# Kernel optimization log

Measured on AMD Instinct MI355X. Metric: run time of the kernel, lower is better.

## Reference

```python
import jax, jax.numpy as jnp
import numpy as np

B, N, DIM = 2, 2048, 512
H, DH = 8, 64            # heads, dim_head; inner_dim = H*DH = 512 == DIM -> to_out is Identity
BAND = 128               # mask keeps -128 <= j-i <= 127
LN_EPS = 1e-5


def _band_mask(n):
    i = jnp.arange(n)
    d = i[None, :] - i[:, None]          # j - i
    return (d >= -BAND) & (d < BAND)     # [n, n] bool


def setup_inputs() -> dict:
    key = jax.random.key(0)
    k1, k2 = jax.random.split(key, 2)
    x = jax.random.normal(k1, (B, N, DIM), dtype=jnp.float32)
    w_qkv = jax.random.normal(k2, (DIM, 3 * H * DH), dtype=jnp.float32) * (DIM ** -0.5)
    gamma = jnp.ones((DIM,), dtype=jnp.float32)
    beta = jnp.zeros((DIM,), dtype=jnp.float32)
    return {"x": x, "w_qkv": w_qkv, "gamma": gamma, "beta": beta}


def reference(x, w_qkv, gamma, beta):
    # LayerNorm
    mu = jnp.mean(x, axis=-1, keepdims=True)
    var = jnp.mean((x - mu) ** 2, axis=-1, keepdims=True)
    xn = (x - mu) * jax.lax.rsqrt(var + LN_EPS) * gamma + beta

    # qkv projection (no bias); split and reshape to [B, H, N, DH]
    qkv = xn @ w_qkv                                   # [B, N, 3*H*DH]
    q, k, v = jnp.split(qkv, 3, axis=-1)
    to_heads = lambda t: t.reshape(B, N, H, DH).transpose(0, 2, 1, 3)
    q, k, v = to_heads(q), to_heads(k), to_heads(v)

    # NOTE: original forward never applies self.scale -> no scaling here (faithful).
    attn = jnp.einsum('bhnd,bhmd->bhnm', q, k)         # [B, H, N, N]
    attn = jnp.where(_band_mask(N), attn, jnp.float32(-10000.0))
    probs = jax.nn.softmax(attn, axis=-1)
    out = jnp.einsum('bhnm,bhmd->bhnd', probs, v)      # [B, H, N, DH]
    out = out.transpose(0, 2, 1, 3).reshape(B, N, H * DH)
    return out  # to_out is Identity since inner_dim == dim
```

## Files before the change

### kernel.cpp

```cpp
#include <hip/hip_runtime.h>
#include <hip/hip_bf16.h>

#define B_    2
#define N_    2048
#define DIM_  512
#define H_    8
#define DH_   64
#define QKVW  1536
#define BAND_ 128
#define LN_EPS 1e-5f

typedef __attribute__((ext_vector_type(8))) short bf16x8;
typedef __attribute__((ext_vector_type(4))) float f32x4;
typedef __attribute__((ext_vector_type(8))) unsigned short ushort8;

__device__ __forceinline__ float bf2f(unsigned short u) {
    union { unsigned int i; float f; } w; w.i = ((unsigned int)u) << 16; return w.f;
}
__device__ __forceinline__ unsigned short f2bf(float f) {
    __hip_bfloat16 h = __float2bfloat16(f);
    return *reinterpret_cast<unsigned short*>(&h);
}
__device__ __forceinline__ void async_copy16(void* lds, const void* g) {
    __builtin_amdgcn_global_load_lds(
        (const __attribute__((address_space(1))) unsigned int*)g,
        (__attribute__((address_space(3))) unsigned int*)lds, 16, 0, 0);
}

__global__ __launch_bounds__(256) void prep_kernel(const float* __restrict__ x,
                                                   const float* __restrict__ gamma,
                                                   const float* __restrict__ beta,
                                                   const float* __restrict__ W,
                                                   unsigned short* __restrict__ xh,
                                                   unsigned short* __restrict__ xl,
                                                   unsigned short* __restrict__ Bh,
                                                   unsigned short* __restrict__ Bl) {
    __shared__ float T[64][65];
    if (blockIdx.x < 1024) {
        const int row  = blockIdx.x * 4 + (threadIdx.x >> 6);
        const int lane = threadIdx.x & 63;
        const float* xr = x + (size_t)row * DIM_ + lane * 8;
        float4 a = *(const float4*)xr;
        float4 c = *(const float4*)(xr + 4);
        float s  = (a.x + a.y) + (a.z + a.w) + (c.x + c.y) + (c.z + c.w);
        float sq = a.x*a.x + a.y*a.y + a.z*a.z + a.w*a.w
                 + c.x*c.x + c.y*c.y + c.z*c.z + c.w*c.w;
        #pragma unroll
        for (int o = 32; o; o >>= 1) { s += __shfl_xor(s, o); sq += __shfl_xor(sq, o); }
        const float mu  = s * (1.0f / DIM_);
        const float var = sq * (1.0f / DIM_) - mu * mu;
        const float rs  = rsqrtf(var + LN_EPS);
        float4 g0 = *(const float4*)(gamma + lane * 8);
        float4 g1 = *(const float4*)(gamma + lane * 8 + 4);
        float4 b0 = *(const float4*)(beta  + lane * 8);
        float4 b1 = *(const float4*)(beta  + lane * 8 + 4);
        const float fv[8] = {
            (a.x - mu) * rs * g0.x + b0.x, (a.y - mu) * rs * g0.y + b0.y,
            (a.z - mu) * rs * g0.z + b0.z, (a.w - mu) * rs * g0.w + b0.w,
            (c.x - mu) * rs * g1.x + b1.x, (c.y - mu) * rs * g1.y + b1.y,
            (c.z - mu) * rs * g1.z + b1.z, (c.w - mu) * rs * g1.w + b1.w };
        ushort8 h, l;
        #pragma unroll
        for (int j = 0; j < 8; ++j) {
            const unsigned short hv = f2bf(fv[j]);
            h[j] = hv; l[j] = f2bf(fv[j] - bf2f(hv));
        }
        *(ushort8*)(xh + (size_t)row * DIM_ + lane * 8) = h;
        *(ushort8*)(xl + (size_t)row * DIM_ + lane * 8) = l;
    } else {
        const int bx = blockIdx.x - 1024;
        const int n0 = (bx % 24) * 64, k0 = (bx / 24) * 64;
        const int tid = threadIdx.x;
        #pragma unroll
        for (int e = 0; e < 4; ++e) {
            const int lin = e * 256 + tid;
            const int kk = lin >> 4;
            const int n4 = (lin & 15) * 4;
            float4 f = *(const float4*)(W + (size_t)(k0 + kk) * QKVW + n0 + n4);
            T[kk][n4 + 0] = f.x; T[kk][n4 + 1] = f.y;
            T[kk][n4 + 2] = f.z; T[kk][n4 + 3] = f.w;
        }
        __syncthreads();
        #pragma unroll
        for (int e = 0; e < 4; ++e) {
            const int lin = e * 256 + tid;
            const int nn = lin >> 4;
            const int kq = (lin & 15) * 4;
            ushort4 h, l;
            float f;
            f = T[kq + 0][nn]; h.x = f2bf(f); l.x = f2bf(f - bf2f(h.x));
            f = T[kq + 1][nn]; h.y = f2bf(f); l.y = f2bf(f - bf2f(h.y));
            f = T[kq + 2][nn]; h.z = f2bf(f); l.z = f2bf(f - bf2f(h.z));
            f = T[kq + 3][nn]; h.w = f2bf(f); l.w = f2bf(f - bf2f(h.w));
            *(ushort4*)(Bh + (size_t)(n0 + nn) * DIM_ + k0 + kq) = h;
            *(ushort4*)(Bl + (size_t)(n0 + nn) * DIM_ + k0 + kq) = l;
        }
    }
}

__global__ __launch_bounds__(256) void gemm_mfma(const unsigned short* __restrict__ Ah,
                                                 const unsigned short* __restrict__ Al,
                                                 const unsigned short* __restrict__ Bh,
                                                 const unsigned short* __restrict__ Bl,
                                                 unsigned short* __restrict__ Qh,
                                                 unsigned short* __restrict__ Ql,
                                                 unsigned short* __restrict__ Kh,
                                                 unsigned short* __restrict__ Kl,
                                                 unsigned short* __restrict__ Vt) {
    __shared__ __attribute__((aligned(16))) unsigned short sAh[64 * 64],  sAl[64 * 64];
    __shared__ __attribute__((aligned(16))) unsigned short sBh[128 * 64], sBl[128 * 64];
    const int tid  = threadIdx.x;
    const int lane = tid & 63, wave = tid >> 6;
    const int wr = wave >> 1, wc = wave & 1;
    const int lg = lane >> 4, l16 = lane & 15;

    const int bid = blockIdx.x;
    const int sb  = (bid & 7) * 96 + (bid >> 3);
    const int row0 = (sb / 12) * 64;
    const int col0 = (sb % 12) * 128;
    const int part = col0 >> 9;

    f32x4 acc[2][4] = {};

    for (int k0 = 0; k0 < DIM_; k0 += 64) {
        __syncthreads();
        #pragma unroll
        for (int e = 0; e < 2; ++e) {
            const int s0  = e * 256 + wave * 64;
            const int idx = s0 + lane;
            const int r   = idx >> 3;
            const int pb  = idx & 7;
            const int klog = pb ^ (r & 7);
            const size_t ga = (size_t)(row0 + r) * DIM_ + k0 + klog * 8;
            async_copy16(&sAh[s0 * 8], Ah + ga);
            if (part < 2) async_copy16(&sAl[s0 * 8], Al + ga);
        }
        #pragma unroll
        for (int e = 0; e < 4; ++e) {
            const int s0  = e * 256 + wave * 64;
            const int idx = s0 + lane;
            const int r   = idx >> 3;
            const int pb  = idx & 7;
            const int klog = pb ^ (r & 7);
            const size_t gb = (size_t)(col0 + r) * DIM_ + k0 + klog * 8;
            async_copy16(&sBh[s0 * 8], Bh + gb);
            if (part < 2) async_copy16(&sBl[s0 * 8], Bl + gb);
        }
        __syncthreads();

        #pragma unroll
        for (int kh = 0; kh < 2; ++kh) {
            bf16x8 ah[2], bh[4];
            #pragma unroll
            for (int mi = 0; mi < 2; ++mi) {
                const int r = wr * 32 + mi * 16 + l16;
                ah[mi] = *(const bf16x8*)&sAh[r * 64 + (((kh * 4 + lg) ^ (r & 7)) * 8)];
            }
            #pragma unroll
            for (int ni = 0; ni < 4; ++ni) {
                const int r = wc * 64 + ni * 16 + l16;
                bh[ni] = *(const bf16x8*)&sBh[r * 64 + (((kh * 4 + lg) ^ (r & 7)) * 8)];
            }
            if (part < 2) {
                bf16x8 al[2], bl[4];
                #pragma unroll
                for (int mi = 0; mi < 2; ++mi) {
                    const int r = wr * 32 + mi * 16 + l16;
                    al[mi] = *(const bf16x8*)&sAl[r * 64 + (((kh * 4 + lg) ^ (r & 7)) * 8)];
                }
                #pragma unroll
                for (int ni = 0; ni < 4; ++ni) {
                    const int r = wc * 64 + ni * 16 + l16;
                    bl[ni] = *(const bf16x8*)&sBl[r * 64 + (((kh * 4 + lg) ^ (r & 7)) * 8)];
                }
                #pragma unroll
                for (int mi = 0; mi < 2; ++mi)
                    #pragma unroll
                    for (int ni = 0; ni < 4; ++ni) {
                        acc[mi][ni] = __builtin_amdgcn_mfma_f32_16x16x32_bf16(ah[mi], bh[ni], acc[mi][ni], 0, 0, 0);
                        acc[mi][ni] = __builtin_amdgcn_mfma_f32_16x16x32_bf16(al[mi], bh[ni], acc[mi][ni], 0, 0, 0);
                        acc[mi][ni] = __builtin_amdgcn_mfma_f32_16x16x32_bf16(ah[mi], bl[ni], acc[mi][ni], 0, 0, 0);
                    }
            } else {
                #pragma unroll
                for (int mi = 0; mi < 2; ++mi)
                    #pragma unroll
                    for (int ni = 0; ni < 4; ++ni)
                        acc[mi][ni] = __builtin_amdgcn_mfma_f32_16x16x32_bf16(ah[mi], bh[ni], acc[mi][ni], 0, 0, 0);
            }
        }
    }

    const int colbase = col0 + wc * 64;
    const int head = (colbase & 511) >> 6;
    if (part < 2) {
        unsigned short* __restrict__ Ih = (part == 0) ? Qh : Kh;
        unsigned short* __restrict__ Il = (part == 0) ? Ql : Kl;
        #pragma unroll
        for (int mi = 0; mi < 2; ++mi) {
            const int rb = row0 + wr * 32 + mi * 16 + lg * 4;
            const int n  = rb & 2047;
            const size_t tbase = ((size_t)((rb >> 11) * H_ + head) * 32 + (n >> 6)) * 4096;
            #pragma unroll
            for (int ni = 0; ni < 4; ++ni) {
                const int d  = ni * 16 + l16;
                const int k8 = d >> 3;
                #pragma unroll
                for (int rr = 0; rr < 4; ++rr) {
                    const int r = (n & 63) + rr;
                    const size_t off = tbase + r * 64 + ((k8 ^ (r & 7)) * 8) + (d & 7);
                    const float v = acc[mi][ni][rr];
                    const unsigned short hv = f2bf(v);
                    Ih[off] = hv;
                    Il[off] = f2bf(v - bf2f(hv));
                }
            }
        }
    } else {
        #pragma unroll
        for (int mi = 0; mi < 2; ++mi) {
            const int rb = row0 + wr * 32 + mi * 16 + lg * 4;
            const int n  = rb & 2047;
            const size_t cbase = ((size_t)((rb >> 11) * H_ + head) * 32 + (n >> 6)) * 4096;
            const int nr = n & 63;
            #pragma unroll
            for (int ni = 0; ni < 4; ++ni) {
                const int d = ni * 16 + l16;
                const size_t off = cbase + d * 64 + (((nr >> 3) ^ (d & 7)) * 8) + (nr & 7);
                ushort4 pk;
                pk.x = f2bf(acc[mi][ni][0]); pk.y = f2bf(acc[mi][ni][1]);
                pk.z = f2bf(acc[mi][ni][2]); pk.w = f2bf(acc[mi][ni][3]);
                *(ushort4*)&Vt[off] = pk;
            }
        }
    }
}

__global__ __launch_bounds__(256) void attn_mfma(const unsigned short* __restrict__ Qh,
                                                 const unsigned short* __restrict__ Ql,
                                                 const unsigned short* __restrict__ Kh,
                                                 const unsigned short* __restrict__ Kl,
                                                 const unsigned short* __restrict__ Vt,
                                                 float* __restrict__ out) {
    const int bid = blockIdx.x;
    const int sb  = (bid & 7) * 64 + (bid >> 3);
    const int tile = sb & 31;
    const int h    = (sb >> 5) & 7;
    const int b    = sb >> 8;
    const int i0   = tile * 64;
    const int tid  = threadIdx.x;
    const int lane = tid & 63, wave = tid >> 6;
    const int lg   = lane >> 4, l16 = lane & 15;

    __shared__ __attribute__((aligned(16))) unsigned short sKh[4096], sKl[4096];
    __shared__ __attribute__((aligned(16))) unsigned short sP[4][1024];

    const size_t hb = (size_t)(b * H_ + h) * 32;

    bf16x8 qh[2], ql[2];
    {
        const int r = wave * 16 + l16;
        const size_t tb = (hb + tile) * 4096;
        #pragma unroll
        for (int kh = 0; kh < 2; ++kh) {
            const size_t off = tb + r * 64 + (((kh * 4 + lg) ^ (r & 7)) * 8);
            qh[kh] = *(const bf16x8*)(Qh + off);
            ql[kh] = *(const bf16x8*)(Ql + off);
        }
    }

    float m_run[4], l_run[4];
    f32x4 oacc[4] = {};
    #pragma unroll
    for (int r = 0; r < 4; ++r) { m_run[r] = -1e30f; l_run[r] = 0.0f; }

    #pragma unroll 1
    for (int c = 0; c < 5; ++c) {
        const int jbase = i0 - 128 + c * 64;
        if (jbase + 64 <= 0 || jbase >= N_) continue;
        __syncthreads();
        const size_t kbG = (hb + (jbase >> 6)) * 4096;
        #pragma unroll
        for (int e = 0; e < 4; ++e) {
            const int s0  = e * 256 + wave * 64;
            const int arr = s0 >> 9;
            const int w0  = (s0 & 511) * 8;
            unsigned short* dst = (arr == 0) ? sKh : sKl;
            const unsigned short* src = (arr == 0) ? Kh : Kl;
            async_copy16(dst + w0, src + kbG + w0 + lane * 8);
        }
        __syncthreads();

        f32x4 sacc[4] = {};
        #pragma unroll
        for (int kh = 0; kh < 2; ++kh) {
            #pragma unroll
            for (int t = 0; t < 4; ++t) {
                const int r = t * 16 + l16;
                const int off = r * 64 + ((((kh * 4 + lg)) ^ (r & 7)) * 8);
                const bf16x8 kbh = *(const bf16x8*)&sKh[off];
                const bf16x8 kbl = *(const bf16x8*)&sKl[off];
                sacc[t] = __builtin_amdgcn_mfma_f32_16x16x32_bf16(qh[kh], kbh, sacc[t], 0, 0, 0);
                sacc[t] = __builtin_amdgcn_mfma_f32_16x16x32_bf16(ql[kh], kbh, sacc[t], 0, 0, 0);
                sacc[t] = __builtin_amdgcn_mfma_f32_16x16x32_bf16(qh[kh], kbl, sacc[t], 0, 0, 0);
            }
        }

        #pragma unroll
        for (int r = 0; r < 4; ++r) {
            const int i = i0 + wave * 16 + lg * 4 + r;
            float sv[4];
            float mx = -1e30f;
            #pragma unroll
            for (int t = 0; t < 4; ++t) {
                const int j = jbase + t * 16 + l16;
                const int d = j - i;
                const bool ok = (d >= -BAND_) && (d < BAND_);
                sv[t] = ok ? sacc[t][r] : -1e30f;
                mx = fmaxf(mx, sv[t]);
            }
            #pragma unroll
            for (int o = 1; o < 16; o <<= 1) mx = fmaxf(mx, __shfl_xor(mx, o));
            const float m_new = fmaxf(m_run[r], mx);
            const float alpha = __expf(m_run[r] - m_new);
            float p[4], lc = 0.f;
            #pragma unroll
            for (int t = 0; t < 4; ++t) { p[t] = __expf(sv[t] - m_new); lc += p[t]; }
            #pragma unroll
            for (int o = 1; o < 16; o <<= 1) lc += __shfl_xor(lc, o);
            l_run[r] = l_run[r] * alpha + lc;
            m_run[r] = m_new;
            #pragma unroll
            for (int dt = 0; dt < 4; ++dt) oacc[dt][r] *= alpha;
            const int q = lg * 4 + r;
            #pragma unroll
            for (int t = 0; t < 4; ++t) {
                const int k = t * 16 + l16;
                sP[wave][q * 64 + (((k >> 3) ^ (q & 7)) * 8) + (k & 7)] = f2bf(p[t]);
            }
        }

        #pragma unroll
        for (int kh = 0; kh < 2; ++kh) {
            const int poff = l16 * 64 + ((((kh * 4 + lg)) ^ (l16 & 7)) * 8);
            const bf16x8 pa = *(const bf16x8*)&sP[wave][poff];
            #pragma unroll
            for (int dt = 0; dt < 4; ++dt) {
                const int rv = dt * 16 + l16;
                const int voff = rv * 64 + ((((kh * 4 + lg)) ^ (rv & 7)) * 8);
                const bf16x8 vb = *(const bf16x8*)(Vt + kbG + voff);
                oacc[dt] = __builtin_amdgcn_mfma_f32_16x16x32_bf16(pa, vb, oacc[dt], 0, 0, 0);
            }
        }
    }

    #pragma unroll
    for (int dt = 0; dt < 4; ++dt)
        #pragma unroll
        for (int r = 0; r < 4; ++r) {
            const int i = i0 + wave * 16 + lg * 4 + r;
            out[((size_t)b * N_ + i) * DIM_ + h * DH_ + dt * 16 + l16] = oacc[dt][r] / l_run[r];
        }
}

extern "C" void kernel_launch(void* const* d_in, const int* in_sizes, int n_in,
                              void* d_out, int out_size, void* d_ws, size_t ws_size,
                              hipStream_t stream) {
    const float* x     = (const float*)d_in[0];
    const float* w     = (const float*)d_in[1];
    const float* gamma = (const float*)d_in[2];
    const float* beta  = (const float*)d_in[3];
    float* out = (float*)d_out;

    const size_t NTOK = (size_t)B_ * N_;
    const size_t IMG  = (size_t)B_ * H_ * 32 * 4096;

    unsigned short* xnh = (unsigned short*)d_ws;
    unsigned short* xnl = xnh + NTOK * DIM_;
    unsigned short* wth = xnl + NTOK * DIM_;
    unsigned short* wtl = wth + (size_t)QKVW * DIM_;
    unsigned short* Qh  = wtl + (size_t)QKVW * DIM_;
    unsigned short* Ql  = Qh + IMG;
    unsigned short* Kh  = Ql + IMG;
    unsigned short* Kl  = Kh + IMG;
    unsigned short* Vt  = Kl + IMG;

    prep_kernel<<<dim3(1024 + 192), dim3(256), 0, stream>>>(x, gamma, beta, w, xnh, xnl, wth, wtl);
    gemm_mfma<<<dim3(768), dim3(256), 0, stream>>>(
        xnh, xnl, wth, wtl, Qh, Ql, Kh, Kl, Vt);
    attn_mfma<<<dim3(512), dim3(256), 0, stream>>>(Qh, Ql, Kh, Kl, Vt, out);
}
```

Baseline: 46.27 us.

## Double-buffer K tiles in LDS to overlap async loads with MFMA compute

Splits the K high/low shared buffers into two stages and prefetches the next 64-key chunk with async global-to-LDS copies while the current chunk is computed. Explicit vmcnt waits and raw s_barrier replace the pair of __syncthreads around each load. The list of valid chunks is precomputed so the loop runs only over the chunks that are in range. This hides global load latency at the cost of doubled LDS for K, which may lower occupancy. It also relies on manual waitcnt counts being correct.

```diff
diff --git a/kernel.cpp b/kernel.cpp
--- a/kernel.cpp
+++ b/kernel.cpp
@@ -252,7 +252,7 @@
     const int lane = tid & 63, wave = tid >> 6;
     const int lg   = lane >> 4, l16 = lane & 15;
 
-    __shared__ __attribute__((aligned(16))) unsigned short sKh[4096], sKl[4096];
+    __shared__ __attribute__((aligned(16))) unsigned short sKh[2][4096], sKl[2][4096];
     __shared__ __attribute__((aligned(16))) unsigned short sP[4][1024];
 
     const size_t hb = (size_t)(b * H_ + h) * 32;
@@ -269,27 +269,45 @@
         }
     }
 
+    int cls[5]; int nc = 0;
+    #pragma unroll
+    for (int c = 0; c < 5; ++c) {
+        const int jb = i0 - 128 + c * 64;
+        if (jb >= 0 && jb < N_) cls[nc++] = jb;
+    }
+
+    auto STAGE = [&](int buf, int jbase) {
+        const size_t kbG = (hb + (jbase >> 6)) * 4096;
+        #pragma unroll
+        for (int e = 0; e < 4; ++e) {
+            const int s0  = e * 256 + wave * 64;
+            const int arr = s0 >> 9;
+            const int w0  = (s0 & 511) * 8;
+            unsigned short* dst = (arr == 0) ? sKh[buf] : sKl[buf];
+            const unsigned short* src = (arr == 0) ? Kh : Kl;
+            async_copy16(dst + w0, src + kbG + w0 + lane * 8);
+        }
+    };
+
     float m_run[4], l_run[4];
     f32x4 oacc[4] = {};
     #pragma unroll
     for (int r = 0; r < 4; ++r) { m_run[r] = -1e30f; l_run[r] = 0.0f; }
 
+    STAGE(0, cls[0]);
     #pragma unroll 1
-    for (int c = 0; c < 5; ++c) {
-        const int jbase = i0 - 128 + c * 64;
-        if (jbase + 64 <= 0 || jbase >= N_) continue;
-        __syncthreads();
+    for (int ci = 0; ci < nc; ++ci) {
+        const int cur = ci & 1;
+        const int jbase = cls[ci];
+        if (ci + 1 < nc) {
+            STAGE(cur ^ 1, cls[ci + 1]);
+            asm volatile("s_waitcnt vmcnt(4)" ::: "memory");
+        } else {
+            asm volatile("s_waitcnt vmcnt(0)" ::: "memory");
+        }
+        __builtin_amdgcn_s_barrier();
+
         const size_t kbG = (hb + (jbase >> 6)) * 4096;
-        #pragma unroll
-        for (int e = 0; e < 4; ++e) {
-            const int s0  = e * 256 + wave * 64;
-            const int arr = s0 >> 9;
-            const int w0  = (s0 & 511) * 8;
-            unsigned short* dst = (arr == 0) ? sKh : sKl;
-            const unsigned short* src = (arr == 0) ? Kh : Kl;
-            async_copy16(dst + w0, src + kbG + w0 + lane * 8);
-        }
-        __syncthreads();
 
         f32x4 sacc[4] = {};
         #pragma unroll
@@ -298,8 +316,8 @@
             for (int t = 0; t < 4; ++t) {
                 const int r = t * 16 + l16;
                 const int off = r * 64 + ((((kh * 4 + lg)) ^ (r & 7)) * 8);
-                const bf16x8 kbh = *(const bf16x8*)&sKh[off];
-                const bf16x8 kbl = *(const bf16x8*)&sKl[off];
+                const bf16x8 kbh = *(const bf16x8*)&sKh[cur][off];
+                const bf16x8 kbl = *(const bf16x8*)&sKl[cur][off];
                 sacc[t] = __builtin_amdgcn_mfma_f32_16x16x32_bf16(qh[kh], kbh, sacc[t], 0, 0, 0);
                 sacc[t] = __builtin_amdgcn_mfma_f32_16x16x32_bf16(ql[kh], kbh, sacc[t], 0, 0, 0);
                 sacc[t] = __builtin_amdgcn_mfma_f32_16x16x32_bf16(qh[kh], kbl, sacc[t], 0, 0, 0);
@@ -352,6 +370,7 @@
                 oacc[dt] = __builtin_amdgcn_mfma_f32_16x16x32_bf16(pa, vb, oacc[dt], 0, 0, 0);
             }
         }
+        __builtin_amdgcn_s_barrier();
     }
 
     #pragma unroll
```

Measured after the change: 46.93 us. Within noise of the previous version (+1.4%).
